# Kernel tuning notes

Hardware: AMD Instinct MI355X
Metric: run time of the kernel (lower is better)

Reference implementation:

```python
import jax, jax.numpy as jnp
import numpy as np

B, P, C, F, E = 8, 65536, 32768, 32, 524288  # batch, n_paths, n_channels, feature, edges


def setup_inputs() -> dict:
    key = jax.random.key(0)
    ks = jax.random.split(key, 8)
    path_features = jax.random.normal(ks[0], (B, P, F), jnp.float32)
    channel_features = jax.random.normal(ks[1], (B, C, F), jnp.float32)
    edge_path = jax.random.randint(ks[2], (E,), 0, P)
    edge_channel = jnp.sort(jax.random.randint(ks[3], (E,), 0, C))
    s = 1.0 / np.sqrt(F)  # PyTorch GRU default init range
    W_ih = jax.random.uniform(ks[4], (3 * F, F), jnp.float32, -s, s)
    W_hh = jax.random.uniform(ks[5], (3 * F, F), jnp.float32, -s, s)
    b_ih = jax.random.uniform(ks[6], (3 * F,), jnp.float32, -s, s)
    b_hh = jax.random.uniform(ks[7], (3 * F,), jnp.float32, -s, s)
    return dict(path_features=path_features, channel_features=channel_features,
                W_ih=W_ih, W_hh=W_hh, b_ih=b_ih, b_hh=b_hh,
                edge_path=edge_path, edge_channel=edge_channel)


def reference(path_features, channel_features, W_ih, W_hh, b_ih, b_hh, edge_path, edge_channel):
    # Ragged per-channel sum of path features (segment-sum over edge list)
    gathered = jnp.swapaxes(path_features[:, edge_path, :], 0, 1)          # [E, B, F]
    agg = jax.ops.segment_sum(gathered, edge_channel, num_segments=C)      # [C, B, F]
    x = jnp.swapaxes(agg, 0, 1)                                            # [B, C, F]
    h = channel_features                                                   # [B, C, F]
    # Single-step GRU (PyTorch gate order: r, z, n)
    gx = x @ W_ih.T + b_ih                                                 # [B, C, 3F]
    gh = h @ W_hh.T + b_hh
    xr, xz, xn = jnp.split(gx, 3, axis=-1)
    hr, hz, hn = jnp.split(gh, 3, axis=-1)
    r = jax.nn.sigmoid(xr + hr)
    z = jax.nn.sigmoid(xz + hz)
    n = jnp.tanh(xn + r * hn)
    return (1.0 - z) * n + z * h                                           # [B, C, F]
```

## Files before the change

### kernel.cpp

```cpp
#include <hip/hip_runtime.h>
#include <hip/hip_fp16.h>

#define NB 8
#define NP 65536
#define NC 32768
#define NF 32
#define NE 524288
#define XROW 40

typedef __attribute__((ext_vector_type(4))) float floatx4;
typedef __attribute__((ext_vector_type(8))) short short8;
typedef __attribute__((ext_vector_type(4))) short short4v;

struct h4 { __half2 lo, hi; };

__device__ __forceinline__ floatx4 h4tof4(h4 v) {
    float2 a = __half22float2(v.lo);
    float2 b = __half22float2(v.hi);
    floatx4 r; r[0] = a.x; r[1] = a.y; r[2] = b.x; r[3] = b.y;
    return r;
}

__device__ __forceinline__ short f2b(float f) {
    union { float f; unsigned int u; } v;
    v.f = f;
    unsigned int lsb = (v.u >> 16) & 1u;
    v.u += 0x7fffu + lsb;
    return (short)(v.u >> 16);
}

__device__ __forceinline__ int lower_bound(const int* __restrict__ a, int v) {
    int lo = 0, hi = NE;
    while (lo < hi) {
        int mid = (lo + hi) >> 1;
        if (a[mid] < v) lo = mid + 1; else hi = mid;
    }
    return lo;
}

__device__ __forceinline__ float sigmoidf_(float v) {
    return 1.f / (1.f + __expf(-v));
}
__device__ __forceinline__ float tanhf_(float v) {
    v = fminf(v, 40.f);
    float t = __expf(2.f * v);
    return (t - 1.f) / (t + 1.f);
}

__global__ __launch_bounds__(256) void transpose_kernel(
    const float* __restrict__ path, __half* __restrict__ pathT)
{
    const int id = blockIdx.x * 256 + threadIdx.x;
    const int f4 = (id & 7) * 4;
    const int b  = (id >> 3) & 7;
    const int p  = id >> 6;
    floatx4 v = *(const floatx4*)(path + ((size_t)b * NP + p) * NF + f4);
    h4 o;
    o.lo = __floats2half2_rn(v[0], v[1]);
    o.hi = __floats2half2_rn(v[2], v[3]);
    *(h4*)(pathT + (size_t)p * (NB * NF) + b * NF + f4) = o;
}

template <int USET>
__global__ __launch_bounds__(256) void fused_gru_kernel(
    const float*  __restrict__ path,
    const __half* __restrict__ pathT,
    const float*  __restrict__ hbuf,
    const float*  __restrict__ W_ih,
    const float*  __restrict__ W_hh,
    const float*  __restrict__ b_ih,
    const float*  __restrict__ b_hh,
    const int*    __restrict__ edge_path,
    const int*    __restrict__ edge_channel,
    float*        __restrict__ out)
{
    const int t    = threadIdx.x;
    const int w    = t >> 6;
    const int lane = t & 63;
    const int cblk = blockIdx.x * 8;

    __shared__ int bounds[9];
    __shared__ __align__(16) short xs [64 * XROW];
    __shared__ __align__(16) short wsx[96 * XROW];
    __shared__ __align__(16) short wsh[96 * XROW];

    if (t < 9) bounds[t] = lower_bound(edge_channel, cblk + t);

    for (int idx = t; idx < 96 * NF; idx += 256) {
        int r = idx >> 5, c = idx & 31;
        wsx[r * XROW + c] = f2b(W_ih[idx]);
        wsh[r * XROW + c] = f2b(W_hh[idx]);
    }
    __syncthreads();

    const int b  = lane >> 3;
    const int fq = lane & 7;
    const float*  prow  = path  + (size_t)b * (NP * NF) + fq * 4;
    const __half* prowT = pathT + b * NF + fq * 4;

    #pragma unroll
    for (int half = 0; half < 2; ++half) {
        const int cl = w * 2 + half;
        const int s = __builtin_amdgcn_readfirstlane(bounds[cl]);
        const int e = __builtin_amdgcn_readfirstlane(bounds[cl + 1]);
        floatx4 acc = {0.f, 0.f, 0.f, 0.f};
        int i = s;
        if (USET) {
            for (; i + 8 <= e; i += 8) {
                int p0 = edge_path[i + 0], p1 = edge_path[i + 1];
                int p2 = edge_path[i + 2], p3 = edge_path[i + 3];
                int p4 = edge_path[i + 4], p5 = edge_path[i + 5];
                int p6 = edge_path[i + 6], p7 = edge_path[i + 7];
                h4 g0 = *(const h4*)(prowT + (size_t)p0 * (NB * NF));
                h4 g1 = *(const h4*)(prowT + (size_t)p1 * (NB * NF));
                h4 g2 = *(const h4*)(prowT + (size_t)p2 * (NB * NF));
                h4 g3 = *(const h4*)(prowT + (size_t)p3 * (NB * NF));
                h4 g4 = *(const h4*)(prowT + (size_t)p4 * (NB * NF));
                h4 g5 = *(const h4*)(prowT + (size_t)p5 * (NB * NF));
                h4 g6 = *(const h4*)(prowT + (size_t)p6 * (NB * NF));
                h4 g7 = *(const h4*)(prowT + (size_t)p7 * (NB * NF));
                acc += ((h4tof4(g0) + h4tof4(g1)) + (h4tof4(g2) + h4tof4(g3)))
                     + ((h4tof4(g4) + h4tof4(g5)) + (h4tof4(g6) + h4tof4(g7)));
            }
            for (; i + 2 <= e; i += 2) {
                int p0 = edge_path[i], p1 = edge_path[i + 1];
                h4 g0 = *(const h4*)(prowT + (size_t)p0 * (NB * NF));
                h4 g1 = *(const h4*)(prowT + (size_t)p1 * (NB * NF));
                acc += h4tof4(g0) + h4tof4(g1);
            }
            if (i < e)
                acc += h4tof4(*(const h4*)(prowT + (size_t)edge_path[i] * (NB * NF)));
        } else {
            for (; i + 8 <= e; i += 8) {
                int p0 = edge_path[i + 0], p1 = edge_path[i + 1];
                int p2 = edge_path[i + 2], p3 = edge_path[i + 3];
                int p4 = edge_path[i + 4], p5 = edge_path[i + 5];
                int p6 = edge_path[i + 6], p7 = edge_path[i + 7];
                floatx4 g0 = *(const floatx4*)(prow + (size_t)p0 * NF);
                floatx4 g1 = *(const floatx4*)(prow + (size_t)p1 * NF);
                floatx4 g2 = *(const floatx4*)(prow + (size_t)p2 * NF);
                floatx4 g3 = *(const floatx4*)(prow + (size_t)p3 * NF);
                floatx4 g4 = *(const floatx4*)(prow + (size_t)p4 * NF);
                floatx4 g5 = *(const floatx4*)(prow + (size_t)p5 * NF);
                floatx4 g6 = *(const floatx4*)(prow + (size_t)p6 * NF);
                floatx4 g7 = *(const floatx4*)(prow + (size_t)p7 * NF);
                acc += ((g0 + g1) + (g2 + g3)) + ((g4 + g5) + (g6 + g7));
            }
            for (; i + 2 <= e; i += 2) {
                int p0 = edge_path[i], p1 = edge_path[i + 1];
                acc += *(const floatx4*)(prow + (size_t)p0 * NF)
                     + *(const floatx4*)(prow + (size_t)p1 * NF);
            }
            if (i < e)
                acc += *(const floatx4*)(prow + (size_t)edge_path[i] * NF);
        }

        short4v xb;
        #pragma unroll
        for (int q = 0; q < 4; ++q) xb[q] = f2b(acc[q]);
        *(short4v*)(&xs[(b * 8 + cl) * XROW + fq * 4]) = xb;
    }
    __syncthreads();

    const int quad = lane >> 4;
    const int n16  = lane & 15;
    const int k0   = quad * 8;

    const int rA = w * 16 + n16;
    short8 ax = *(const short8*)(&xs[rA * XROW + k0]);

    const int bA = rA >> 3;
    const int cA = cblk + (rA & 7);
    const float* hrow = hbuf + ((size_t)bA * NC + cA) * NF + k0;
    floatx4 h0 = *(const floatx4*)(hrow);
    floatx4 h1 = *(const floatx4*)(hrow + 4);
    short8 ah;
    #pragma unroll
    for (int q = 0; q < 4; ++q) { ah[q] = f2b(h0[q]); ah[4 + q] = f2b(h1[q]); }

    float bxv[6], bhv[6];
    #pragma unroll
    for (int tt = 0; tt < 6; ++tt) {
        bxv[tt] = b_ih[16 * tt + n16];
        bhv[tt] = b_hh[16 * tt + n16];
    }

    const floatx4 zero = {0.f, 0.f, 0.f, 0.f};
    floatx4 g[4];
    #pragma unroll
    for (int tt = 0; tt < 4; ++tt) {
        short8 bw = *(const short8*)(&wsx[(16 * tt + n16) * XROW + k0]);
        floatx4 a = __builtin_amdgcn_mfma_f32_16x16x32_bf16(ax, bw, zero, 0, 0, 0);
        bw = *(const short8*)(&wsh[(16 * tt + n16) * XROW + k0]);
        g[tt] = __builtin_amdgcn_mfma_f32_16x16x32_bf16(ah, bw, a, 0, 0, 0);
    }
    floatx4 nx[2], nh[2];
    #pragma unroll
    for (int u = 0; u < 2; ++u) {
        const int tt = 4 + u;
        short8 bw = *(const short8*)(&wsx[(16 * tt + n16) * XROW + k0]);
        nx[u] = __builtin_amdgcn_mfma_f32_16x16x32_bf16(ax, bw, zero, 0, 0, 0);
        bw = *(const short8*)(&wsh[(16 * tt + n16) * XROW + k0]);
        nh[u] = __builtin_amdgcn_mfma_f32_16x16x32_bf16(ah, bw, zero, 0, 0, 0);
    }

    #pragma unroll
    for (int i = 0; i < 4; ++i) {
        const int r  = w * 16 + quad * 4 + i;
        const int b2 = r >> 3;
        const size_t m = (size_t)b2 * NC + (cblk + (r & 7));
        float r0 = sigmoidf_(g[0][i] + bxv[0] + bhv[0]);
        float r1 = sigmoidf_(g[1][i] + bxv[1] + bhv[1]);
        float z0 = sigmoidf_(g[2][i] + bxv[2] + bhv[2]);
        float z1 = sigmoidf_(g[3][i] + bxv[3] + bhv[3]);
        float n0 = tanhf_(nx[0][i] + bxv[4] + r0 * (nh[0][i] + bhv[4]));
        float n1 = tanhf_(nx[1][i] + bxv[5] + r1 * (nh[1][i] + bhv[5]));
        float hv0 = hbuf[m * NF + n16];
        float hv1 = hbuf[m * NF + 16 + n16];
        out[m * NF + n16]      = (1.f - z0) * n0 + z0 * hv0;
        out[m * NF + 16 + n16] = (1.f - z1) * n1 + z1 * hv1;
    }
}

extern "C" void kernel_launch(void* const* d_in, const int* in_sizes, int n_in,
                              void* d_out, int out_size, void* d_ws, size_t ws_size,
                              hipStream_t stream) {
    const float* path = (const float*)d_in[0];
    const float* chan = (const float*)d_in[1];
    const float* W_ih = (const float*)d_in[2];
    const float* W_hh = (const float*)d_in[3];
    const float* b_ih = (const float*)d_in[4];
    const float* b_hh = (const float*)d_in[5];
    const int* edge_path    = (const int*)d_in[6];
    const int* edge_channel = (const int*)d_in[7];
    float* out = (float*)d_out;

    const size_t needT = (size_t)NP * NB * NF * sizeof(__half);
    if (ws_size >= needT) {
        __half* pathT = (__half*)d_ws;
        transpose_kernel<<<dim3((NP * NB * NF / 4) / 256), dim3(256), 0, stream>>>(
            path, pathT);
        fused_gru_kernel<1><<<dim3(NC / 8), dim3(256), 0, stream>>>(
            path, pathT, chan, W_ih, W_hh, b_ih, b_hh, edge_path, edge_channel, out);
    } else {
        fused_gru_kernel<0><<<dim3(NC / 8), dim3(256), 0, stream>>>(
            path, (const __half*)nullptr, chan, W_ih, W_hh, b_ih, b_hh,
            edge_path, edge_channel, out);
    }
}
```

Before: 222.3 us.

## Merge per-wave channel gathers into one 16-wide loop with half-precision pair adds

Each wave now walks the edge range of both of its channels in a single loop, issuing 16 gather loads at a time. The loads are routed to one of two accumulators, with a slow per-edge path only for the group that straddles the channel boundary. Pairs of gathered values are added in fp16 before widening, which cuts conversion and add work but adds rounding error. The transpose kernel also handles 8 features per thread instead of 4, so it launches fewer threads and issues wider stores.

Result: no change. 219.0 us (-1.5%).

```diff
diff --git a/kernel.cpp b/kernel.cpp
--- a/kernel.cpp
+++ b/kernel.cpp
@@ -13,6 +13,7 @@
 typedef __attribute__((ext_vector_type(4))) short short4v;
 
 struct h4 { __half2 lo, hi; };
+struct h8 { __half2 a, b, c, d; };
 
 __device__ __forceinline__ floatx4 h4tof4(h4 v) {
     float2 a = __half22float2(v.lo);
@@ -51,14 +52,18 @@
     const float* __restrict__ path, __half* __restrict__ pathT)
 {
     const int id = blockIdx.x * 256 + threadIdx.x;
-    const int f4 = (id & 7) * 4;
-    const int b  = (id >> 3) & 7;
-    const int p  = id >> 6;
-    floatx4 v = *(const floatx4*)(path + ((size_t)b * NP + p) * NF + f4);
-    h4 o;
-    o.lo = __floats2half2_rn(v[0], v[1]);
-    o.hi = __floats2half2_rn(v[2], v[3]);
-    *(h4*)(pathT + (size_t)p * (NB * NF) + b * NF + f4) = o;
+    const int fh = id & 3;
+    const int b  = (id >> 2) & 7;
+    const int p  = id >> 5;
+    const float* src = path + ((size_t)b * NP + p) * NF + fh * 8;
+    floatx4 v0 = *(const floatx4*)(src);
+    floatx4 v1 = *(const floatx4*)(src + 4);
+    h8 o;
+    o.a = __floats2half2_rn(v0[0], v0[1]);
+    o.b = __floats2half2_rn(v0[2], v0[3]);
+    o.c = __floats2half2_rn(v1[0], v1[1]);
+    o.d = __floats2half2_rn(v1[2], v1[3]);
+    *(h8*)(pathT + (size_t)p * (NB * NF) + b * NF + fh * 8) = o;
 }
 
 template <int USET>
@@ -98,39 +103,63 @@
     const float*  prow  = path  + (size_t)b * (NP * NF) + fq * 4;
     const __half* prowT = pathT + b * NF + fq * 4;
 
-    #pragma unroll
-    for (int half = 0; half < 2; ++half) {
-        const int cl = w * 2 + half;
-        const int s = __builtin_amdgcn_readfirstlane(bounds[cl]);
-        const int e = __builtin_amdgcn_readfirstlane(bounds[cl + 1]);
-        floatx4 acc = {0.f, 0.f, 0.f, 0.f};
-        int i = s;
-        if (USET) {
-            for (; i + 8 <= e; i += 8) {
-                int p0 = edge_path[i + 0], p1 = edge_path[i + 1];
-                int p2 = edge_path[i + 2], p3 = edge_path[i + 3];
-                int p4 = edge_path[i + 4], p5 = edge_path[i + 5];
-                int p6 = edge_path[i + 6], p7 = edge_path[i + 7];
-                h4 g0 = *(const h4*)(prowT + (size_t)p0 * (NB * NF));
-                h4 g1 = *(const h4*)(prowT + (size_t)p1 * (NB * NF));
-                h4 g2 = *(const h4*)(prowT + (size_t)p2 * (NB * NF));
-                h4 g3 = *(const h4*)(prowT + (size_t)p3 * (NB * NF));
-                h4 g4 = *(const h4*)(prowT + (size_t)p4 * (NB * NF));
-                h4 g5 = *(const h4*)(prowT + (size_t)p5 * (NB * NF));
-                h4 g6 = *(const h4*)(prowT + (size_t)p6 * (NB * NF));
-                h4 g7 = *(const h4*)(prowT + (size_t)p7 * (NB * NF));
-                acc += ((h4tof4(g0) + h4tof4(g1)) + (h4tof4(g2) + h4tof4(g3)))
-                     + ((h4tof4(g4) + h4tof4(g5)) + (h4tof4(g6) + h4tof4(g7)));
+    floatx4 acc0 = {0.f, 0.f, 0.f, 0.f};
+    floatx4 acc1 = {0.f, 0.f, 0.f, 0.f};
+
+    if (USET) {
+        const int s0  = __builtin_amdgcn_readfirstlane(bounds[w * 2]);
+        const int mid = __builtin_amdgcn_readfirstlane(bounds[w * 2 + 1]);
+        const int e1  = __builtin_amdgcn_readfirstlane(bounds[w * 2 + 2]);
+
+        auto gulp16 = [&](int base, floatx4& acc) {
+            int p[16];
+            #pragma unroll
+            for (int k = 0; k < 16; ++k) p[k] = edge_path[base + k];
+            h4 g[16];
+            #pragma unroll
+            for (int k = 0; k < 16; ++k)
+                g[k] = *(const h4*)(prowT + (size_t)p[k] * (NB * NF));
+            floatx4 s = acc;
+            #pragma unroll
+            for (int k = 0; k < 8; ++k) {
+                __half2 lo = __hadd2(g[2 * k].lo, g[2 * k + 1].lo);
+                __half2 hi = __hadd2(g[2 * k].hi, g[2 * k + 1].hi);
+                float2 fa = __half22float2(lo);
+                float2 fb = __half22float2(hi);
+                floatx4 v; v[0] = fa.x; v[1] = fa.y; v[2] = fb.x; v[3] = fb.y;
+                s += v;
             }
-            for (; i + 2 <= e; i += 2) {
-                int p0 = edge_path[i], p1 = edge_path[i + 1];
-                h4 g0 = *(const h4*)(prowT + (size_t)p0 * (NB * NF));
-                h4 g1 = *(const h4*)(prowT + (size_t)p1 * (NB * NF));
-                acc += h4tof4(g0) + h4tof4(g1);
+            acc = s;
+        };
+
+        int i = s0;
+        while (i + 16 <= e1) {
+            if (i >= mid) {
+                gulp16(i, acc1);
+            } else if (i + 16 <= mid) {
+                gulp16(i, acc0);
+            } else {
+                #pragma unroll
+                for (int k = 0; k < 16; ++k) {
+                    floatx4 v = h4tof4(
+                        *(const h4*)(prowT + (size_t)edge_path[i + k] * (NB * NF)));
+                    if (i + k < mid) acc0 += v; else acc1 += v;
+                }
             }
-            if (i < e)
-                acc += h4tof4(*(const h4*)(prowT + (size_t)edge_path[i] * (NB * NF)));
-        } else {
+            i += 16;
+        }
+        for (; i < e1; ++i) {
+            floatx4 v = h4tof4(
+                *(const h4*)(prowT + (size_t)edge_path[i] * (NB * NF)));
+            if (i < mid) acc0 += v; else acc1 += v;
+        }
+    } else {
+        #pragma unroll
+        for (int half = 0; half < 2; ++half) {
+            const int s = __builtin_amdgcn_readfirstlane(bounds[w * 2 + half]);
+            const int e = __builtin_amdgcn_readfirstlane(bounds[w * 2 + half + 1]);
+            floatx4 acc = {0.f, 0.f, 0.f, 0.f};
+            int i = s;
             for (; i + 8 <= e; i += 8) {
                 int p0 = edge_path[i + 0], p1 = edge_path[i + 1];
                 int p2 = edge_path[i + 2], p3 = edge_path[i + 3];
@@ -146,19 +175,18 @@
                 floatx4 g7 = *(const floatx4*)(prow + (size_t)p7 * NF);
                 acc += ((g0 + g1) + (g2 + g3)) + ((g4 + g5) + (g6 + g7));
             }
-            for (; i + 2 <= e; i += 2) {
-                int p0 = edge_path[i], p1 = edge_path[i + 1];
-                acc += *(const floatx4*)(prow + (size_t)p0 * NF)
-                     + *(const floatx4*)(prow + (size_t)p1 * NF);
-            }
-            if (i < e)
+            for (; i < e; ++i)
                 acc += *(const floatx4*)(prow + (size_t)edge_path[i] * NF);
+            if (half == 0) acc0 = acc; else acc1 = acc;
         }
-
-        short4v xb;
+    }
+
+    {
+        short4v xb0, xb1;
         #pragma unroll
-        for (int q = 0; q < 4; ++q) xb[q] = f2b(acc[q]);
-        *(short4v*)(&xs[(b * 8 + cl) * XROW + fq * 4]) = xb;
+        for (int q = 0; q < 4; ++q) { xb0[q] = f2b(acc0[q]); xb1[q] = f2b(acc1[q]); }
+        *(short4v*)(&xs[(b * 8 + w * 2)     * XROW + fq * 4]) = xb0;
+        *(short4v*)(&xs[(b * 8 + w * 2 + 1) * XROW + fq * 4]) = xb1;
     }
     __syncthreads();
 
@@ -238,7 +266,7 @@
     const size_t needT = (size_t)NP * NB * NF * sizeof(__half);
     if (ws_size >= needT) {
         __half* pathT = (__half*)d_ws;
-        transpose_kernel<<<dim3((NP * NB * NF / 4) / 256), dim3(256), 0, stream>>>(
+        transpose_kernel<<<dim3((NP * NB * 4) / 256), dim3(256), 0, stream>>>(
             path, pathT);
         fused_gru_kernel<1><<<dim3(NC / 8), dim3(256), 0, stream>>>(
             path, pathT, chan, W_ih, W_hh, b_ih, b_hh, edge_path, edge_channel, out);
```
